# Performance work log

Hardware: AMD Instinct MI355X
Metric: run time of the kernel (lower is better)

Reference implementation:

```python
import jax, jax.numpy as jnp
import numpy as np

EPS = 1e-5

def _ln(x, g, b):
    m = jnp.mean(x, axis=-1, keepdims=True)
    v = jnp.var(x, axis=-1, keepdims=True)
    return (x - m) / jnp.sqrt(v + EPS) * g + b

def _mha(q, k, v, Wqkv, bqkv, Wo, bo, nh):
    # torch nn.MultiheadAttention with packed in_proj: rows [0:D]=Q, [D:2D]=K, [2D:3D]=V
    D = q.shape[-1]; hd = D // nh
    qp = q @ Wqkv[:D].T + bqkv[:D]
    kp = k @ Wqkv[D:2 * D].T + bqkv[D:2 * D]
    vp = v @ Wqkv[2 * D:].T + bqkv[2 * D:]
    sh = lambda t: t.reshape(t.shape[0], t.shape[1], nh, hd).transpose(0, 2, 1, 3)
    scores = jnp.einsum('bhqd,bhkd->bhqk', sh(qp), sh(kp)) / np.float32(np.sqrt(hd))
    a = jax.nn.softmax(scores, axis=-1)
    o = jnp.einsum('bhqk,bhkd->bhqd', a, sh(vp)).transpose(0, 2, 1, 3).reshape(q.shape[0], q.shape[1], D)
    return o @ Wo.T + bo

def _forward(x, W_in, b_in, W_l, b_l, g_l, be_l, W_ih, W_hh, b_ih, b_hh, mem0,
             W_rh, b_rh, W_wh, b_wh, W_eh, b_eh, W_rg, b_rg, W_wg, b_wg,
             W_wm_qkv, b_wm_qkv, W_wm_o, b_wm_o, W_ca_qkv, b_ca_qkv, W_ca_o, b_ca_o,
             W_ai, b_ai, g_ca, be_ca, W_out, b_out):
    B, S, _ = x.shape
    H = W_in.shape[0]
    # input projection + residual MLP stack (eval mode: dropout is identity)
    h = x @ W_in.T + b_in
    for i in range(W_l.shape[0]):
        r = h
        h = _ln(jax.nn.relu(h @ W_l[i].T + b_l[i]), g_l[i], be_l[i])
        h = h + r  # use_residual=True
    # working-memory (NTM-style) scan over time
    Hd = H

    def step(carry, xt):
        hs, cs, mem = carry
        gates = xt @ W_ih.T + b_ih + hs @ W_hh.T + b_hh
        i_, f_, g_, o_ = jnp.split(gates, 4, axis=-1)  # torch LSTM gate order i,f,g,o
        cs = jax.nn.sigmoid(f_) * cs + jax.nn.sigmoid(i_) * jnp.tanh(g_)
        hs = jax.nn.sigmoid(o_) * jnp.tanh(cs)
        # read (attention over memory, then gate)
        rk = hs @ W_rh.T + b_rh
        ro = _mha(rk[:, None, :], mem, mem, W_wm_qkv, b_wm_qkv, W_wm_o, b_wm_o, 4)
        rg = jax.nn.sigmoid(hs @ W_rg.T + b_rg)  # [B,1]
        read = (rg[:, :, None] * ro)[:, 0]
        # write (erase + add with content-based addressing, unscaled bmm softmax)
        wp = hs @ W_wh.T + b_wh
        wk, wv = wp[:, :Hd], wp[:, Hd:]
        ev = jax.nn.sigmoid(hs @ W_eh.T + b_eh)
        wg = jax.nn.sigmoid(hs @ W_wg.T + b_wg)  # [B,1]
        att = jax.nn.softmax(jnp.einsum('bd,bmd->bm', wk, mem), axis=-1)
        ew = att[:, :, None]  # [B,M,1]
        mem = mem * (1.0 - ew * ev[:, None, :]) + wg[:, None, :] * (ew * wv[:, None, :])
        return (hs, cs, mem), xt + read

    mem_init = jnp.broadcast_to(mem0, (B,) + mem0.shape)
    init = (jnp.zeros((B, H), x.dtype), jnp.zeros((B, H), x.dtype), mem_init)
    _, outs = jax.lax.scan(step, init, h.transpose(1, 0, 2))
    wm = outs.transpose(1, 0, 2)  # [B,S,H]
    # cognitive attention, task_type='general' (no task modulation branch)
    att = _mha(wm, wm, wm, W_ca_qkv, b_ca_qkv, W_ca_o, b_ca_o, 8)
    inten = jax.nn.sigmoid(wm @ W_ai.T + b_ai)
    co = _ln(att * inten + wm, g_ca, be_ca)
    return co @ W_out.T + b_out

def setup_inputs():
    key = jax.random.key(0)
    ks = iter(jax.random.split(key, 40))
    B, S, DI, H, DO, L, M = 16, 512, 64, 128, 64, 3, 32
    w = lambda *s: jax.random.normal(next(ks), s, jnp.float32) * 0.05
    d = {}
    d['x'] = jax.random.normal(next(ks), (B, S, DI), jnp.float32)
    d['W_in'] = w(H, DI); d['b_in'] = jnp.zeros(H)
    d['W_l'] = w(L, H, H); d['b_l'] = jnp.zeros((L, H))
    d['g_l'] = jnp.ones((L, H)); d['be_l'] = jnp.zeros((L, H))
    d['W_ih'] = w(4 * H, H); d['W_hh'] = w(4 * H, H)
    d['b_ih'] = jnp.zeros(4 * H); d['b_hh'] = jnp.zeros(4 * H)
    d['mem0'] = w(M, H)
    d['W_rh'] = w(H, H); d['b_rh'] = jnp.zeros(H)
    d['W_wh'] = w(2 * H, H); d['b_wh'] = jnp.zeros(2 * H)
    d['W_eh'] = w(H, H); d['b_eh'] = jnp.zeros(H)
    d['W_rg'] = w(1, H); d['b_rg'] = jnp.zeros(1)
    d['W_wg'] = w(1, H); d['b_wg'] = jnp.zeros(1)
    d['W_wm_qkv'] = w(3 * H, H); d['b_wm_qkv'] = jnp.zeros(3 * H)
    d['W_wm_o'] = w(H, H); d['b_wm_o'] = jnp.zeros(H)
    d['W_ca_qkv'] = w(3 * H, H); d['b_ca_qkv'] = jnp.zeros(3 * H)
    d['W_ca_o'] = w(H, H); d['b_ca_o'] = jnp.zeros(H)
    d['W_ai'] = w(1, H); d['b_ai'] = jnp.zeros(1)
    d['g_ca'] = jnp.ones(H); d['be_ca'] = jnp.zeros(H)
    d['W_out'] = w(DO, H); d['b_out'] = jnp.zeros(DO)
    return d

def reference(x, W_in, b_in, W_l, b_l, g_l, be_l, W_ih, W_hh, b_ih, b_hh, mem0,
              W_rh, b_rh, W_wh, b_wh, W_eh, b_eh, W_rg, b_rg, W_wg, b_wg,
              W_wm_qkv, b_wm_qkv, W_wm_o, b_wm_o, W_ca_qkv, b_ca_qkv, W_ca_o, b_ca_o,
              W_ai, b_ai, g_ca, be_ca, W_out, b_out):
    return _forward(x, W_in, b_in, W_l, b_l, g_l, be_l, W_ih, W_hh, b_ih, b_hh, mem0,
                    W_rh, b_rh, W_wh, b_wh, W_eh, b_eh, W_rg, b_rg, W_wg, b_wg,
                    W_wm_qkv, b_wm_qkv, W_wm_o, b_wm_o, W_ca_qkv, b_ca_qkv, W_ca_o, b_ca_o,
                    W_ai, b_ai, g_ca, be_ca, W_out, b_out)
```

## Files before the change

kernel.cpp:

```cpp
#include <hip/hip_runtime.h>
#include <hip/hip_bf16.h>


typedef short bf16x8 __attribute__((ext_vector_type(8)));
typedef float f32x4 __attribute__((ext_vector_type(4)));
typedef float f32x16 __attribute__((ext_vector_type(16)));

__device__ __forceinline__ float bl(uint u) { return __uint_as_float(u << 16); }
__device__ __forceinline__ float bh(uint u) { return __uint_as_float(u & 0xffff0000u); }
__device__ __forceinline__ float b2f(ushort u) { return __uint_as_float(((uint)u) << 16); }
__device__ __forceinline__ ushort f2b(float f) {
  uint u = __float_as_uint(f);
  u += 0x7fffu + ((u >> 16) & 1u);
  return (ushort)(u >> 16);
}
__device__ __forceinline__ uint cvtpk(float lo, float hi) {
  uint r;
  asm("v_cvt_pk_bf16_f32 %0, %1, %2" : "=v"(r) : "v"(lo), "v"(hi));
  return r;
}
__device__ __forceinline__ float rdl(float v, int lane) {
  return __int_as_float(__builtin_amdgcn_readlane(__float_as_int(v), lane));
}
__device__ __forceinline__ float sigm(float x) { return 1.0f / (1.0f + __expf(-x)); }
__device__ __forceinline__ float tanh_(float x) { float e = __expf(2.0f * x); return 1.0f - 2.0f / (e + 1.0f); }

__device__ __forceinline__ float dppror_add(float v, const int n) {
  int s;
  switch (n) {
    case 1: s = __builtin_amdgcn_update_dpp(0, __float_as_int(v), 0x121, 0xF, 0xF, true); break;
    case 2: s = __builtin_amdgcn_update_dpp(0, __float_as_int(v), 0x122, 0xF, 0xF, true); break;
    case 4: s = __builtin_amdgcn_update_dpp(0, __float_as_int(v), 0x124, 0xF, 0xF, true); break;
    default: s = __builtin_amdgcn_update_dpp(0, __float_as_int(v), 0x128, 0xF, 0xF, true); break;
  }
  return v + __int_as_float(s);
}
__device__ __forceinline__ float dppror_max(float v, const int n) {
  int s;
  switch (n) {
    case 1: s = __builtin_amdgcn_update_dpp(0, __float_as_int(v), 0x121, 0xF, 0xF, true); break;
    case 2: s = __builtin_amdgcn_update_dpp(0, __float_as_int(v), 0x122, 0xF, 0xF, true); break;
    case 4: s = __builtin_amdgcn_update_dpp(0, __float_as_int(v), 0x124, 0xF, 0xF, true); break;
    default: s = __builtin_amdgcn_update_dpp(0, __float_as_int(v), 0x128, 0xF, 0xF, true); break;
  }
  return fmaxf(v, __int_as_float(s));
}
__device__ __forceinline__ float swz16(float v) {
  return __int_as_float(__builtin_amdgcn_ds_swizzle(__float_as_int(v), 0x401F));
}
__device__ __forceinline__ float fold32_add(float v) {
  int a = __float_as_int(v), b = a;
  asm("v_permlane32_swap_b32 %0, %1" : "+v"(a), "+v"(b));
  return __int_as_float(a) + __int_as_float(b);
}

#define O_H     ((size_t)0)
#define O_GX    ((size_t)1048576)
#define O_EW    ((size_t)1048576)
#define O_QCA   ((size_t)1048576)
#define O_KCA   ((size_t)2097152)
#define O_VCA   ((size_t)3145728)
#define O_AO    ((size_t)4194304)
#define O_HS    ((size_t)5242880)
#define O_WM    ((size_t)5242880)
#define O_ST    ((size_t)6291456)
#define O_Q     ((size_t)9437184)
#define O_WGS   ((size_t)10485760)
#define O_RGS   ((size_t)10493952)
#define O_BQC   ((size_t)10502144)
#define O_MEMA  ((size_t)10502272)
#define O_PWIN  ((size_t)27279488)
#define O_PWL   ((size_t)27283584)
#define O_PWIH  ((size_t)27308160)
#define O_PCMB  ((size_t)27340928)
#define O_PQKV  ((size_t)27373696)
#define O_PWOC  ((size_t)27398272)
#define O_PWOUT ((size_t)27406464)
#define O_PWOWM ((size_t)27410688)
#define O_WQC16 ((size_t)27418880)
#define O_CAN   ((size_t)27427072)

#define F4LD(DST, OFS, P) { float4 _f = *(const float4*)(P); DST[(OFS)]=_f.x; DST[(OFS)+1]=_f.y; DST[(OFS)+2]=_f.z; DST[(OFS)+3]=_f.w; }

struct CV { const void* src; uint dst; uint n; };
struct CVA { CV d[36]; };
__global__ __launch_bounds__(256) void k_cvt(CVA a, ushort* cb)
{
  __shared__ int flag;
  int tid = threadIdx.x;
  const ushort* xu = (const ushort*)a.d[0].src;
  if (tid < 64) {
    int sane = 0;
    for (int i = tid; i < 512; i += 64) {
      int e = (xu[2 * i] >> 7) & 0xFF;
      sane += (e >= 0x70 && e <= 0x8E) ? 1 : 0;
    }
#pragma unroll
    for (int d = 1; d < 64; d <<= 1) sane += __shfl_xor(sane, d, 64);
    if (tid == 0) flag = (sane > 256) ? 0 : 1;
  }
  __syncthreads();
  int isf32 = flag;
  CV c = a.d[blockIdx.x];
  ushort* dst = cb + c.dst;
  uint start = blockIdx.y * 256 + tid, stride = gridDim.y * 256;
  if (isf32) {
    const float* s = (const float*)c.src;
    for (uint j = start; j < c.n; j += stride) dst[j] = f2b(s[j]);
  } else {
    const ushort* s = (const ushort*)c.src;
    for (uint j = start; j < c.n; j += stride) dst[j] = s[j];
  }
}

__global__ __launch_bounds__(256) void k_wqcomb(const ushort* __restrict__ Wqkv, const ushort* __restrict__ Wrh,
                                                const ushort* __restrict__ brh, const ushort* __restrict__ bqkv,
                                                ushort* __restrict__ wqc, float* __restrict__ bqc)
{
  __shared__ float qr[2][128];
  int tid = threadIdx.x;
  int r = tid >> 7, e = tid & 127;
  int j = blockIdx.x * 2 + r;
  qr[r][e] = b2f(Wqkv[j * 128 + e]);
  __syncthreads();
  float acc = 0.f;
  for (int k = 0; k < 128; ++k) acc += qr[r][k] * b2f(Wrh[k * 128 + e]);
  wqc[j * 128 + e] = f2b(acc);
  if (e == 0) {
    float s = 0.f;
    for (int k = 0; k < 128; ++k) s += qr[r][k] * b2f(brh[k]);
    bqc[j] = s + b2f(bqkv[j]);
  }
}

struct PD { const ushort* src; uint* dst; int R, C2, RT, base; };
struct PA { PD d[12]; };
__global__ __launch_bounds__(256) void k_pack(PA a)
{
  int p = blockIdx.x >> 5, sl = blockIdx.x & 31;
  PD q = a.d[p];
  for (int d2 = sl; d2 < q.C2; d2 += 32)
    for (int j = threadIdx.x; j < q.R; j += 256)
      q.dst[(size_t)d2 * q.RT + q.base + j] = *(const uint*)(q.src + (size_t)j * q.C2 * 2 + d2 * 2);
}

__device__ __forceinline__ void mlp_layer(float& h0, float& h1, const uint* wp, const float* bias, int li, int l)
{
  float t0 = bias[(1 + li) * 128 + l], t1 = bias[(1 + li) * 128 + 64 + l];
#pragma unroll
  for (int d2 = 0; d2 < 64; ++d2) {
    float s0 = rdl(d2 < 32 ? h0 : h1, (2 * d2) & 63);
    float s1 = rdl(d2 < 32 ? h0 : h1, (2 * d2 + 1) & 63);
    uint u0 = wp[d2 * 128 + l], u1 = wp[d2 * 128 + 64 + l];
    t0 += s0 * bl(u0) + s1 * bh(u0);
    t1 += s0 * bl(u1) + s1 * bh(u1);
  }
  t0 = fmaxf(t0, 0.f); t1 = fmaxf(t1, 0.f);
  float sm = t0 + t1, sq = t0 * t0 + t1 * t1;
#pragma unroll
  for (int d = 1; d < 64; d <<= 1) { sm += __shfl_xor(sm, d, 64); sq += __shfl_xor(sq, d, 64); }
  float mn = sm * 0.0078125f;
  float var = sq * 0.0078125f - mn * mn;
  float rstd = rsqrtf(var + 1e-5f);
  float ng0 = bias[(4 + li) * 128 + l], ng1 = bias[(4 + li) * 128 + 64 + l];
  float nb0 = bias[(7 + li) * 128 + l], nb1 = bias[(7 + li) * 128 + 64 + l];
  h0 = (t0 - mn) * rstd * ng0 + nb0 + h0;
  h1 = (t1 - mn) * rstd * ng1 + nb1 + h1;
}

__global__ __launch_bounds__(256, 1) void k_mlp(const ushort* __restrict__ x, const uint* __restrict__ pk,
    const ushort* __restrict__ b_in, const ushort* __restrict__ b_l, const ushort* __restrict__ g_l,
    const ushort* __restrict__ be_l, float* __restrict__ h_all)
{
  __shared__ uint lds[12288];
  __shared__ float bias[1280];
  int tid = threadIdx.x;
  for (int i = tid; i < 12288; i += 256) lds[i] = pk[i];
  for (int i = tid; i < 1280; i += 256) {
    int which = i >> 7, e = i & 127;
    float v;
    if (which == 0) v = b2f(b_in[e]);
    else if (which < 4) v = b2f(b_l[(which - 1) * 128 + e]);
    else if (which < 7) v = b2f(g_l[(which - 4) * 128 + e]);
    else v = b2f(be_l[(which - 7) * 128 + e]);
    bias[i] = v;
  }
  __syncthreads();
  int wv = tid >> 6, l = tid & 63;
  float h0a[8], h1a[8];
#pragma unroll
  for (int ps = 0; ps < 8; ++ps) {
    int tok = blockIdx.x * 32 + ps * 4 + wv;
    float xv = b2f(x[(size_t)tok * 64 + l]);
    float h0 = bias[l], h1 = bias[64 + l];
#pragma unroll
    for (int d2 = 0; d2 < 32; ++d2) {
      float s0 = rdl(xv, 2 * d2), s1 = rdl(xv, 2 * d2 + 1);
      uint u0 = lds[d2 * 128 + l], u1 = lds[d2 * 128 + 64 + l];
      h0 += s0 * bl(u0) + s1 * bh(u0);
      h1 += s0 * bl(u1) + s1 * bh(u1);
    }
    mlp_layer(h0, h1, lds + 4096, bias, 0, l);
    h0a[ps] = h0; h1a[ps] = h1;
  }
  __syncthreads();
  for (int i = tid; i < 8192; i += 256) lds[i] = pk[12288 + i];
  __syncthreads();
#pragma unroll
  for (int ps = 0; ps < 8; ++ps) {
    float h0 = h0a[ps], h1 = h1a[ps];
    mlp_layer(h0, h1, lds, bias, 1, l);
    h0a[ps] = h0; h1a[ps] = h1;
  }
  __syncthreads();
  for (int i = tid; i < 8192; i += 256) lds[i] = pk[20480 + i];
  __syncthreads();
#pragma unroll
  for (int ps = 0; ps < 8; ++ps) {
    int tok = blockIdx.x * 32 + ps * 4 + wv;
    float h0 = h0a[ps], h1 = h1a[ps];
    mlp_layer(h0, h1, lds, bias, 2, l);
    h_all[(size_t)tok * 128 + l] = h0;
    h_all[(size_t)tok * 128 + 64 + l] = h1;
  }
}

__global__ __launch_bounds__(256, 1) void k_gates(const float* __restrict__ h_all, const uint* __restrict__ pk,
    const ushort* __restrict__ b_ih, const ushort* __restrict__ b_hh, float* __restrict__ gx)
{
  __shared__ uint lds[8192];
  __shared__ float biasg[512];
  int tid = threadIdx.x;
  for (int i = tid; i < 512; i += 256) biasg[i] = b2f(b_ih[i]) + b2f(b_hh[i]);
  int wv = tid >> 6, l = tid & 63;
  for (int s = 0; s < 4; ++s) {
    __syncthreads();
    for (int i = tid; i < 8192; i += 256) { int d2 = i >> 7, j = i & 127; lds[i] = pk[d2 * 512 + s * 128 + j]; }
    __syncthreads();
    for (int ps = 0; ps < 8; ++ps) {
      int tok = blockIdx.x * 32 + ps * 4 + wv;
      float h0 = h_all[(size_t)tok * 128 + l], h1 = h_all[(size_t)tok * 128 + 64 + l];
      float a0 = biasg[s * 128 + l], a1 = biasg[s * 128 + 64 + l];
#pragma unroll
      for (int d2 = 0; d2 < 64; ++d2) {
        float s0 = rdl(d2 < 32 ? h0 : h1, (2 * d2) & 63);
        float s1 = rdl(d2 < 32 ? h0 : h1, (2 * d2 + 1) & 63);
        uint u0 = lds[d2 * 128 + l], u1 = lds[d2 * 128 + 64 + l];
        a0 += s0 * bl(u0) + s1 * bh(u0);
        a1 += s0 * bl(u1) + s1 * bh(u1);
      }
      gx[(size_t)tok * 512 + s * 128 + l] = a0;
      gx[(size_t)tok * 512 + s * 128 + 64 + l] = a1;
    }
  }
}

__global__ __launch_bounds__(512, 2) void k_lstm(const float* __restrict__ gx, const ushort* __restrict__ Whh,
                                                 float* __restrict__ hs_all)
{
  __shared__ float hsl[128];
  __shared__ float gact[512];
  int tid = threadIdx.x;
  int b = blockIdx.x;
  float2 w2[64];
  {
    const ushort* rp = Whh + (size_t)tid * 128;
#pragma unroll
    for (int q = 0; q < 16; ++q) {
      uint4 v = *(const uint4*)(rp + q * 8);
      w2[q * 4 + 0] = make_float2(bl(v.x), bh(v.x));
      w2[q * 4 + 1] = make_float2(bl(v.y), bh(v.y));
      w2[q * 4 + 2] = make_float2(bl(v.z), bh(v.z));
      w2[q * 4 + 3] = make_float2(bl(v.w), bh(v.w));
    }
  }
  if (tid < 128) hsl[tid] = 0.f;
  float cs = 0.f;
  const float* gbase = gx + (size_t)b * 512 * 512;
  float gcur = gbase[tid];
  int grp = tid >> 7;
  __syncthreads();
  for (int t = 0; t < 512; ++t) {
    float gnext = 0.f;
    if (t < 511) gnext = gbase[(size_t)(t + 1) * 512 + tid];
    float ax = gcur, ay = 0.f;
#pragma unroll
    for (int i = 0; i < 64; ++i) {
      float2 s2 = *(const float2*)(hsl + 2 * i);
      ax = fmaf(w2[i].x, s2.x, ax);
      ay = fmaf(w2[i].y, s2.y, ay);
    }
    float a = ax + ay;
    gact[tid] = (grp == 2) ? tanh_(a) : sigm(a);
    __syncthreads();
    if (tid < 128) {
      float si = gact[tid], sf = gact[128 + tid], tg = gact[256 + tid], so = gact[384 + tid];
      cs = sf * cs + si * tg;
      float hv = so * tanh_(cs);
      hsl[tid] = hv;
      hs_all[((size_t)b * 512 + t) * 128 + tid] = hv;
    }
    gcur = gnext;
    __syncthreads();
  }
}

__global__ __launch_bounds__(256, 1) void k_proj(const float* __restrict__ hs_all, const uint* __restrict__ pk,
    const ushort* __restrict__ bwh, const ushort* __restrict__ beh, const float* __restrict__ bqc,
    const ushort* __restrict__ wrg, const ushort* __restrict__ brg, const ushort* __restrict__ wwg,
    const ushort* __restrict__ bwg,
    float* __restrict__ st, float* __restrict__ q_a, float* __restrict__ rg_a)
{
  __shared__ uint lds[8192];
  __shared__ float biasc[512];
  int tid = threadIdx.x;
  for (int i = tid; i < 512; i += 256)
    biasc[i] = (i < 256) ? b2f(bwh[i]) : (i < 384) ? b2f(beh[i - 256]) : bqc[i - 384];
  float brgv = b2f(brg[0]), bwgv = b2f(bwg[0]);
  int wv = tid >> 6, l = tid & 63;
  for (int s = 0; s < 4; ++s) {
    __syncthreads();
    for (int i = tid; i < 8192; i += 256) { int d2 = i >> 7, j = i & 127; lds[i] = pk[d2 * 512 + s * 128 + j]; }
    __syncthreads();
    for (int ps = 0; ps < 8; ++ps) {
      int tok = blockIdx.x * 32 + ps * 4 + wv;
      float h0 = hs_all[(size_t)tok * 128 + l], h1 = hs_all[(size_t)tok * 128 + 64 + l];
      float a0 = biasc[s * 128 + l], a1 = biasc[s * 128 + 64 + l];
#pragma unroll
      for (int d2 = 0; d2 < 64; ++d2) {
        float s0 = rdl(d2 < 32 ? h0 : h1, (2 * d2) & 63);
        float s1 = rdl(d2 < 32 ? h0 : h1, (2 * d2 + 1) & 63);
        uint u0 = lds[d2 * 128 + l], u1 = lds[d2 * 128 + 64 + l];
        a0 += s0 * bl(u0) + s1 * bh(u0);
        a1 += s0 * bl(u1) + s1 * bh(u1);
      }
      if (s == 0) {
        st[(size_t)tok * 384 + l] = a0;
        st[(size_t)tok * 384 + 64 + l] = a1;
        float pr = h0 * b2f(wrg[l]) + h1 * b2f(wrg[64 + l]);
#pragma unroll
        for (int d = 1; d < 64; d <<= 1) pr += __shfl_xor(pr, d, 64);
        if (l == 0) rg_a[tok] = sigm(pr + brgv);
      } else if (s == 1) {
        float pw = h0 * b2f(wwg[l]) + h1 * b2f(wwg[64 + l]);
#pragma unroll
        for (int d = 1; d < 64; d <<= 1) pw += __shfl_xor(pw, d, 64);
        float wg = sigm(pw + bwgv);
        st[(size_t)tok * 384 + 256 + l] = wg * a0;
        st[(size_t)tok * 384 + 256 + 64 + l] = wg * a1;
      } else if (s == 2) {
        st[(size_t)tok * 384 + 128 + l] = sigm(a0);
        st[(size_t)tok * 384 + 128 + 64 + l] = sigm(a1);
      } else {
        q_a[(size_t)tok * 128 + l] = a0;
        q_a[(size_t)tok * 128 + 64 + l] = a1;
      }
    }
  }
}

__global__ __launch_bounds__(64, 1) void k_memrec(const float* __restrict__ st, const ushort* __restrict__ mem0,
    float* __restrict__ ew_all)
{
  __shared__ __align__(16) float sbuf[2][384];
  int l = threadIdx.x;
  int b = blockIdx.x;
  int r = l & 31, h = l >> 5;
  f32x16 mA, mB, mC, mD;
  {
    const uint* m0 = (const uint*)mem0 + r * 64 + 32 * h;
    uint4 uq;
#define LD16(V, OFS) \
    uq = *(const uint4*)(m0 + (OFS)); \
    V[0]=bl(uq.x); V[1]=bh(uq.x); V[2]=bl(uq.y); V[3]=bh(uq.y); \
    V[4]=bl(uq.z); V[5]=bh(uq.z); V[6]=bl(uq.w); V[7]=bh(uq.w); \
    uq = *(const uint4*)(m0 + (OFS) + 4); \
    V[8]=bl(uq.x); V[9]=bh(uq.x); V[10]=bl(uq.y); V[11]=bh(uq.y); \
    V[12]=bl(uq.z); V[13]=bh(uq.z); V[14]=bl(uq.w); V[15]=bh(uq.w);
    LD16(mA, 0) LD16(mB, 8) LD16(mC, 16) LD16(mD, 24)
#undef LD16
  }
  const float* stb = st + (size_t)b * 512 * 384;
  {
    float4 a = *(const float4*)(stb + 4 * l);
    float2 c = *(const float2*)(stb + 256 + 2 * l);
    *(float4*)(&sbuf[0][4 * l]) = a;
    *(float2*)(&sbuf[0][256 + 2 * l]) = c;
  }
  float moff = 0.f;
  float* ewp = ew_all + (size_t)b * 512 * 32 + r;
  for (int t = 0; t < 512; ++t) {
    int cur = t & 1, nxt = cur ^ 1;
    float4 ga = make_float4(0.f, 0.f, 0.f, 0.f);
    float2 gc = make_float2(0.f, 0.f);
    if (t < 511) {
      const float* sp = stb + (size_t)(t + 1) * 384;
      ga = *(const float4*)(sp + 4 * l);
      gc = *(const float2*)(sp + 256 + 2 * l);
    }
    const float* wkp = &sbuf[cur][h * 64];
    float dx = 0.f, dy = 0.f, dz = 0.f, dw = 0.f;
    float4 w4;
#define DOT4(V, J0, OFS) \
    w4 = *(const float4*)(wkp + (OFS)); \
    dx = fmaf(w4.x, V[(J0)+0], dx); dy = fmaf(w4.y, V[(J0)+1], dy); \
    dz = fmaf(w4.z, V[(J0)+2], dz); dw = fmaf(w4.w, V[(J0)+3], dw);
    DOT4(mA, 0, 0)  DOT4(mA, 4, 4)  DOT4(mA, 8, 8)   DOT4(mA, 12, 12)
    DOT4(mB, 0, 16) DOT4(mB, 4, 20) DOT4(mB, 8, 24)  DOT4(mB, 12, 28)
    DOT4(mC, 0, 32) DOT4(mC, 4, 36) DOT4(mC, 8, 40)  DOT4(mC, 12, 44)
    DOT4(mD, 0, 48) DOT4(mD, 4, 52) DOT4(mD, 8, 56)  DOT4(mD, 12, 60)
#undef DOT4
    float dp = (dx + dy) + (dz + dw);
    dp = fold32_add(dp);
    float e = __expf(dp - moff);
    float s16 = dppror_add(dppror_add(dppror_add(dppror_add(e, 1), 2), 4), 8);
    float den = s16 + swz16(s16);
    float ew = e / den;
    float x16 = dppror_max(dppror_max(dppror_max(dppror_max(dp, 1), 2), 4), 8);
    const float* evp = &sbuf[cur][128 + h * 64];
    const float* gvp = &sbuf[cur][256 + h * 64];
    float4 e4, g4;
#define UPD4(V, J0, OFS) \
    e4 = *(const float4*)(evp + (OFS)); g4 = *(const float4*)(gvp + (OFS)); \
    V[(J0)+0] = fmaf(ew, fmaf(-e4.x, V[(J0)+0], g4.x), V[(J0)+0]); \
    V[(J0)+1] = fmaf(ew, fmaf(-e4.y, V[(J0)+1], g4.y), V[(J0)+1]); \
    V[(J0)+2] = fmaf(ew, fmaf(-e4.z, V[(J0)+2], g4.z), V[(J0)+2]); \
    V[(J0)+3] = fmaf(ew, fmaf(-e4.w, V[(J0)+3], g4.w), V[(J0)+3]);
    UPD4(mA, 0, 0)  UPD4(mA, 4, 4)  UPD4(mA, 8, 8)   UPD4(mA, 12, 12)
    UPD4(mB, 0, 16) UPD4(mB, 4, 20) UPD4(mB, 8, 24)  UPD4(mB, 12, 28)
    UPD4(mC, 0, 32) UPD4(mC, 4, 36) UPD4(mC, 8, 40)  UPD4(mC, 12, 44)
    UPD4(mD, 0, 48) UPD4(mD, 4, 52) UPD4(mD, 8, 56)  UPD4(mD, 12, 60)
#undef UPD4
    if (t < 511) {
      *(float4*)(&sbuf[nxt][4 * l]) = ga;
      *(float2*)(&sbuf[nxt][256 + 2 * l]) = gc;
    }
    if (l < 32) ewp[(size_t)t * 32] = ew;
    moff = fmaxf(x16, swz16(x16));
  }
}

__global__ __launch_bounds__(256, 1) void k_snap(const float* __restrict__ st, const float* __restrict__ ew_all,
    const ushort* __restrict__ mem0, uint* __restrict__ mem_all)
{
  int b = blockIdx.x >> 3;
  int j = ((blockIdx.x & 7) << 8) + threadIdx.x;
  int m = j >> 6, d2 = j & 63;
  uint u0 = ((const uint*)mem0)[(m << 6) + d2];
  float s0 = bl(u0), s1 = bh(u0);
  const float* ep = st + (size_t)b * 512 * 384 + 128 + 2 * d2;
  const float* gp = ep + 128;
  const float* ap = ew_all + (size_t)b * 512 * 32 + m;
  uint* mb = mem_all + (size_t)b * 512 * 2048 + (m << 6) + d2;
  for (int t = 0; t < 512; t += 4) {
    float2 eA = *(const float2*)(ep + (size_t)(t + 0) * 384);
    float2 eB = *(const float2*)(ep + (size_t)(t + 1) * 384);
    float2 eC = *(const float2*)(ep + (size_t)(t + 2) * 384);
    float2 eD = *(const float2*)(ep + (size_t)(t + 3) * 384);
    float2 gA = *(const float2*)(gp + (size_t)(t + 0) * 384);
    float2 gB = *(const float2*)(gp + (size_t)(t + 1) * 384);
    float2 gC = *(const float2*)(gp + (size_t)(t + 2) * 384);
    float2 gD = *(const float2*)(gp + (size_t)(t + 3) * 384);
    float a0 = ap[(size_t)(t + 0) * 32];
    float a1 = ap[(size_t)(t + 1) * 32];
    float a2 = ap[(size_t)(t + 2) * 32];
    float a3 = ap[(size_t)(t + 3) * 32];
    mb[(size_t)(t + 0) * 2048] = cvtpk(s0, s1);
    s0 = fmaf(a0, fmaf(-eA.x, s0, gA.x), s0);
    s1 = fmaf(a0, fmaf(-eA.y, s1, gA.y), s1);
    mb[(size_t)(t + 1) * 2048] = cvtpk(s0, s1);
    s0 = fmaf(a1, fmaf(-eB.x, s0, gB.x), s0);
    s1 = fmaf(a1, fmaf(-eB.y, s1, gB.y), s1);
    mb[(size_t)(t + 2) * 2048] = cvtpk(s0, s1);
    s0 = fmaf(a2, fmaf(-eC.x, s0, gC.x), s0);
    s1 = fmaf(a2, fmaf(-eC.y, s1, gC.y), s1);
    mb[(size_t)(t + 3) * 2048] = cvtpk(s0, s1);
    s0 = fmaf(a3, fmaf(-eD.x, s0, gD.x), s0);
    s1 = fmaf(a3, fmaf(-eD.y, s1, gD.y), s1);
  }
}

__global__ __launch_bounds__(256, 1) void k_read(const ushort* __restrict__ Wqkv, const ushort* __restrict__ bwo,
    const uint* __restrict__ wo_pk, const uint* __restrict__ mem_all, const float* __restrict__ q_all,
    const float* __restrict__ rg_all, const float* __restrict__ h_all, float* __restrict__ wm_all)
{
  __shared__ float Kl[32 * 133];
  __shared__ float Vl[32 * 133];
  __shared__ __align__(16) char ml[8192];
  __shared__ float ql[128];
  __shared__ float ol[128];
  __shared__ float part[256];
  int tid = threadIdx.x, l = tid & 63, w = tid >> 6;
  int b = blockIdx.x >> 6, c = blockIdx.x & 63;
  int mat = w >> 1, chh = w & 1;
  bf16x8 bfr[4][4];
#pragma unroll
  for (int ct = 0; ct < 4; ++ct)
#pragma unroll
    for (int kt = 0; kt < 4; ++kt) {
      int j = chh * 64 + ct * 16 + (l & 15);
      bfr[ct][kt] = *(const bf16x8*)(Wqkv + (size_t)(128 + mat * 128 + j) * 128 + kt * 32 + (l >> 4) * 8);
    }
  for (int s8 = 0; s8 < 8; ++s8) {
    int t = c * 8 + s8;
    size_t bt = (size_t)b * 512 + t;
    {
      const uint4* src = (const uint4*)(mem_all + bt * 2048);
      uint4 v0 = src[tid * 2], v1 = src[tid * 2 + 1];
      int row = tid >> 3;
      int b0 = row * 256 + (tid & 7) * 32;
      int sw = (row & 7) << 4;
      *(uint4*)(ml + (b0 ^ sw)) = v0;
      *(uint4*)(ml + ((b0 + 16) ^ sw)) = v1;
    }
    if (tid < 128) ql[tid] = q_all[bt * 128 + tid];
    __syncthreads();
    f32x4 acc[2][4];
#pragma unroll
    for (int rt = 0; rt < 2; ++rt)
#pragma unroll
      for (int ct = 0; ct < 4; ++ct) { f32x4 z = {0.f, 0.f, 0.f, 0.f}; acc[rt][ct] = z; }
    bf16x8 af[2][4];
#pragma unroll
    for (int rt = 0; rt < 2; ++rt)
#pragma unroll
      for (int kt = 0; kt < 4; ++kt) {
        int row = rt * 16 + (l & 15);
        int byte0 = (row * 256 + kt * 64 + (l >> 4) * 16) ^ ((row & 7) << 4);
        af[rt][kt] = *(const bf16x8*)(ml + byte0);
      }
#pragma unroll
    for (int rt = 0; rt < 2; ++rt)
#pragma unroll
      for (int ct = 0; ct < 4; ++ct)
#pragma unroll
        for (int kt = 0; kt < 4; ++kt)
          acc[rt][ct] = __builtin_amdgcn_mfma_f32_16x16x32_bf16(af[rt][kt], bfr[ct][kt], acc[rt][ct], 0, 0, 0);
    {
      float* dst = mat ? Vl : Kl;
#pragma unroll
      for (int rt = 0; rt < 2; ++rt)
#pragma unroll
        for (int ct = 0; ct < 4; ++ct)
#pragma unroll
          for (int rr = 0; rr < 4; ++rr) {
            int row = rt * 16 + (l >> 4) * 4 + rr;
            int col = chh * 64 + ct * 16 + (l & 15);
            dst[row * 133 + col] = acc[rt][ct][rr];
          }
    }
    __syncthreads();
    {
      int hh = w;
      float qv[16];
#pragma unroll
      for (int q = 0; q < 4; ++q) { F4LD(qv, 4 * q, ql + hh * 32 + (l >> 5) * 16 + 4 * q); }
      int m = l & 31;
      float sv = 0.f;
#pragma unroll
      for (int i = 0; i < 16; ++i) sv += qv[i] * Kl[m * 133 + hh * 32 + (l >> 5) * 16 + i];
      sv += __shfl_xor(sv, 32, 64);
      sv *= 0.1767766952966369f;
      float mx = sv;
      mx = fmaxf(mx, __shfl_xor(mx, 1, 64)); mx = fmaxf(mx, __shfl_xor(mx, 2, 64));
      mx = fmaxf(mx, __shfl_xor(mx, 4, 64)); mx = fmaxf(mx, __shfl_xor(mx, 8, 64));
      mx = fmaxf(mx, __shfl_xor(mx, 16, 64));
      float e = __expf(sv - mx);
      float den = e;
      den += __shfl_xor(den, 1, 64); den += __shfl_xor(den, 2, 64); den += __shfl_xor(den, 4, 64);
      den += __shfl_xor(den, 8, 64); den += __shfl_xor(den, 16, 64);
      float a = e / den;
      float o = 0.f;
      int dpos = l & 31, mh = l >> 5;
#pragma unroll
      for (int i = 0; i < 16; ++i) {
        int mm = mh * 16 + i;
        float am = __shfl(a, mm, 64);
        o += am * Vl[mm * 133 + hh * 32 + dpos];
      }
      o += __shfl_xor(o, 32, 64);
      if (l < 32) ol[hh * 32 + dpos] = o;
    }
    __syncthreads();
    {
      int j = tid & 127, dh = tid >> 7;
      float o0 = ol[l], o1 = ol[64 + l];
      float pa = 0.f;
#pragma unroll
      for (int i2 = 0; i2 < 32; ++i2) {
        int d2 = dh * 32 + i2;
        float s0, s1;
        if (dh == 0) { s0 = rdl(o0, 2 * i2); s1 = rdl(o0, 2 * i2 + 1); }
        else { s0 = rdl(o1, 2 * i2); s1 = rdl(o1, 2 * i2 + 1); }
        uint u = wo_pk[d2 * 128 + j];
        pa += s0 * bl(u) + s1 * bh(u);
      }
      part[tid] = pa;
    }
    __syncthreads();
    if (tid < 128) {
      float ro = part[tid] + part[tid + 128] + b2f(bwo[tid]);
      float rg = rg_all[bt];
      wm_all[bt * 128 + tid] = h_all[bt * 128 + tid] + rg * ro;
    }
    __syncthreads();
  }
}

__global__ __launch_bounds__(256, 1) void k_caqkv(const float* __restrict__ wm, const uint* __restrict__ pk,
    const ushort* __restrict__ bqkv, float* __restrict__ qca, float* __restrict__ kca, float* __restrict__ vca)
{
  __shared__ uint lds[8192];
  int tid = threadIdx.x;
  int wv = tid >> 6, l = tid & 63;
  for (int s = 0; s < 3; ++s) {
    __syncthreads();
    for (int i = tid; i < 8192; i += 256) { int d2 = i >> 7, j = i & 127; lds[i] = pk[d2 * 384 + s * 128 + j]; }
    __syncthreads();
    for (int ps = 0; ps < 8; ++ps) {
      int tok = blockIdx.x * 32 + ps * 4 + wv;
      int b = tok >> 9, ss = tok & 511;
      float h0 = wm[(size_t)tok * 128 + l], h1 = wm[(size_t)tok * 128 + 64 + l];
      float a0 = b2f(bqkv[s * 128 + l]), a1 = b2f(bqkv[s * 128 + 64 + l]);
#pragma unroll
      for (int d2 = 0; d2 < 64; ++d2) {
        float s0 = rdl(d2 < 32 ? h0 : h1, (2 * d2) & 63);
        float s1 = rdl(d2 < 32 ? h0 : h1, (2 * d2 + 1) & 63);
        uint u0 = lds[d2 * 128 + l], u1 = lds[d2 * 128 + 64 + l];
        a0 += s0 * bl(u0) + s1 * bh(u0);
        a1 += s0 * bl(u1) + s1 * bh(u1);
      }
#pragma unroll
      for (int k = 0; k < 2; ++k) {
        int j = l + 64 * k;
        int hd = j >> 4, dd = j & 15;
        size_t idx = ((size_t)(b * 8 + hd) * 512 + ss) * 16 + dd;
        float v = k == 0 ? a0 : a1;
        if (s == 0) qca[idx] = v * 0.25f;
        else if (s == 1) kca[idx] = v;
        else vca[idx] = v;
      }
    }
  }
}

__global__ __launch_bounds__(256, 1) void k_caattn(const float* __restrict__ qca, const float* __restrict__ kca,
    const float* __restrict__ vca, float* __restrict__ ao)
{
  __shared__ float kl[8192];
  __shared__ uint vl[4096];
  int tid = threadIdx.x;
  int bh_ = blockIdx.x >> 1, half = blockIdx.x & 1;
  for (int i = tid; i < 8192; i += 256) kl[i] = kca[(size_t)bh_ * 8192 + i];
  for (int i = tid; i < 4096; i += 256) {
    float v0 = vca[(size_t)bh_ * 8192 + 2 * i], v1 = vca[(size_t)bh_ * 8192 + 2 * i + 1];
    vl[i] = (uint)f2b(v0) | ((uint)f2b(v1) << 16);
  }
  __syncthreads();
  int r = half * 256 + tid;
  float qv[16];
#pragma unroll
  for (int q = 0; q < 4; ++q) { F4LD(qv, 4 * q, qca + (size_t)bh_ * 8192 + r * 16 + 4 * q); }
  float o[16];
#pragma unroll
  for (int i = 0; i < 16; ++i) o[i] = 0.f;
  float mx = -3e38f, den = 0.f;
  for (int ch = 0; ch < 8; ++ch) {
    float sc[64];
#pragma unroll
    for (int m2 = 0; m2 < 64; ++m2) {
      const float* kr = kl + (ch * 64 + m2) * 16;
      float s = 0.f;
#pragma unroll
      for (int i = 0; i < 16; ++i) s += qv[i] * kr[i];
      sc[m2] = s;
    }
    float cm = sc[0];
#pragma unroll
    for (int m2 = 1; m2 < 64; ++m2) cm = fmaxf(cm, sc[m2]);
    if (cm > mx) {
      float rs = __expf(mx - cm);
      den *= rs;
#pragma unroll
      for (int i = 0; i < 16; ++i) o[i] *= rs;
      mx = cm;
    }
#pragma unroll
    for (int m2 = 0; m2 < 64; ++m2) {
      float e = __expf(sc[m2] - mx);
      den += e;
      const uint* vr = vl + (ch * 64 + m2) * 8;
#pragma unroll
      for (int i = 0; i < 8; ++i) {
        uint u = vr[i];
        o[2 * i] += e * bl(u);
        o[2 * i + 1] += e * bh(u);
      }
    }
  }
  float rd = 1.f / den;
#pragma unroll
  for (int q = 0; q < 4; ++q) {
    float4 f = make_float4(o[4 * q] * rd, o[4 * q + 1] * rd, o[4 * q + 2] * rd, o[4 * q + 3] * rd);
    *(float4*)(ao + (size_t)bh_ * 8192 + r * 16 + 4 * q) = f;
  }
}

__global__ __launch_bounds__(256, 1) void k_cafinal(const float* __restrict__ wm, const float* __restrict__ ao,
    const uint* __restrict__ pko, const uint* __restrict__ pkout,
    const ushort* __restrict__ wai, const ushort* __restrict__ bai, const ushort* __restrict__ gca,
    const ushort* __restrict__ beca, const ushort* __restrict__ boca, const ushort* __restrict__ bout,
    float* __restrict__ out)
{
  __shared__ uint lds[12288];
  __shared__ float fb[576];
  int tid = threadIdx.x;
  for (int i = tid; i < 8192; i += 256) lds[i] = pko[i];
  for (int i = tid; i < 4096; i += 256) lds[8192 + i] = pkout[i];
  for (int i = tid; i < 576; i += 256) {
    float v;
    if (i < 128) v = b2f(wai[i]);
    else if (i < 256) v = b2f(gca[i - 128]);
    else if (i < 384) v = b2f(beca[i - 256]);
    else if (i < 512) v = b2f(boca[i - 384]);
    else v = b2f(bout[i - 512]);
    fb[i] = v;
  }
  __syncthreads();
  float baiv = b2f(bai[0]);
  int wv = tid >> 6, l = tid & 63;
  for (int ps = 0; ps < 8; ++ps) {
    int tok = blockIdx.x * 32 + ps * 4 + wv;
    int b = tok >> 9, s = tok & 511;
    float w0 = wm[(size_t)tok * 128 + l], w1 = wm[(size_t)tok * 128 + 64 + l];
    float o0 = ao[((size_t)(b * 8 + (l >> 4)) * 512 + s) * 16 + (l & 15)];
    float o1 = ao[((size_t)(b * 8 + 4 + (l >> 4)) * 512 + s) * 16 + (l & 15)];
    float ip = w0 * fb[l] + w1 * fb[64 + l];
#pragma unroll
    for (int d = 1; d < 64; d <<= 1) ip += __shfl_xor(ip, d, 64);
    float it = sigm(ip + baiv);
    float a0 = fb[384 + l], a1 = fb[384 + 64 + l];
#pragma unroll
    for (int d2 = 0; d2 < 64; ++d2) {
      float s0 = rdl(d2 < 32 ? o0 : o1, (2 * d2) & 63);
      float s1 = rdl(d2 < 32 ? o0 : o1, (2 * d2 + 1) & 63);
      uint u0 = lds[d2 * 128 + l], u1 = lds[d2 * 128 + 64 + l];
      a0 += s0 * bl(u0) + s1 * bh(u0);
      a1 += s0 * bl(u1) + s1 * bh(u1);
    }
    float x0 = a0 * it + w0, x1 = a1 * it + w1;
    float smv = x0 + x1, sq = x0 * x0 + x1 * x1;
#pragma unroll
    for (int d = 1; d < 64; d <<= 1) { smv += __shfl_xor(smv, d, 64); sq += __shfl_xor(sq, d, 64); }
    float mn = smv * 0.0078125f;
    float var = sq * 0.0078125f - mn * mn;
    float rstd = rsqrtf(var + 1e-5f);
    float c0 = (x0 - mn) * rstd * fb[128 + l] + fb[256 + l];
    float c1 = (x1 - mn) * rstd * fb[128 + 64 + l] + fb[256 + 64 + l];
    float ob = fb[512 + l];
#pragma unroll
    for (int d2 = 0; d2 < 64; ++d2) {
      float s0 = rdl(d2 < 32 ? c0 : c1, (2 * d2) & 63);
      float s1 = rdl(d2 < 32 ? c0 : c1, (2 * d2 + 1) & 63);
      uint u = lds[8192 + d2 * 64 + l];
      ob += s0 * bl(u) + s1 * bh(u);
    }
    out[(size_t)tok * 64 + l] = ob;
  }
}

extern "C" void kernel_launch(void* const* d_in, const int* in_sizes, int n_in,
                              void* d_out, int out_size, void* d_ws, size_t ws_size,
                              hipStream_t stream)
{
  (void)out_size; (void)ws_size;
  float* ws = (float*)d_ws;
  uint* wsu = (uint*)d_ws;
  ushort* cb = (ushort*)(wsu + O_CAN);

  uint off[36]; uint cum = 0;
  for (int i = 0; i < 36; ++i) { off[i] = cum; cum = (cum + (uint)in_sizes[i] + 7u) & ~7u; }

  CVA ca;
  for (int i = 0; i < 36; ++i) ca.d[i] = CV{ d_in[i], off[i], (uint)in_sizes[i] };
  k_cvt<<<dim3(36, 16), 256, 0, stream>>>(ca, cb);

  const ushort* x        = cb + off[0];
  const ushort* W_in     = cb + off[1];
  const ushort* b_in     = cb + off[2];
  const ushort* W_l      = cb + off[3];
  const ushort* b_l      = cb + off[4];
  const ushort* g_l      = cb + off[5];
  const ushort* be_l     = cb + off[6];
  const ushort* W_ih     = cb + off[7];
  const ushort* W_hh     = cb + off[8];
  const ushort* b_ih     = cb + off[9];
  const ushort* b_hh     = cb + off[10];
  const ushort* mem0     = cb + off[11];
  const ushort* W_rh     = cb + off[12];
  const ushort* b_rh     = cb + off[13];
  const ushort* W_wh     = cb + off[14];
  const ushort* b_wh     = cb + off[15];
  const ushort* W_eh     = cb + off[16];
  const ushort* b_eh     = cb + off[17];
  const ushort* W_rg     = cb + off[18];
  const ushort* b_rg     = cb + off[19];
  const ushort* W_wg     = cb + off[20];
  const ushort* b_wg     = cb + off[21];
  const ushort* W_wm_qkv = cb + off[22];
  const ushort* b_wm_qkv = cb + off[23];
  const ushort* W_wm_o   = cb + off[24];
  const ushort* b_wm_o   = cb + off[25];
  const ushort* W_ca_qkv = cb + off[26];
  const ushort* b_ca_qkv = cb + off[27];
  const ushort* W_ca_o   = cb + off[28];
  const ushort* b_ca_o   = cb + off[29];
  const ushort* W_ai     = cb + off[30];
  const ushort* b_ai     = cb + off[31];
  const ushort* g_ca     = cb + off[32];
  const ushort* be_ca    = cb + off[33];
  const ushort* W_out    = cb + off[34];
  const ushort* b_out    = cb + off[35];

  k_wqcomb<<<64, 256, 0, stream>>>(W_wm_qkv, W_rh, b_rh, b_wm_qkv, (ushort*)(wsu + O_WQC16), ws + O_BQC);

  PA pa;
  pa.d[0]  = PD{ W_in,                       wsu + O_PWIN,  128, 32, 128, 0 };
  pa.d[1]  = PD{ W_l,                        wsu + O_PWL,   128, 64, 128, 0 };
  pa.d[2]  = PD{ W_l + 16384,                wsu + O_PWL + 8192,  128, 64, 128, 0 };
  pa.d[3]  = PD{ W_l + 32768,                wsu + O_PWL + 16384, 128, 64, 128, 0 };
  pa.d[4]  = PD{ W_ih,                       wsu + O_PWIH,  512, 64, 512, 0 };
  pa.d[5]  = PD{ W_wh,                       wsu + O_PCMB,  256, 64, 512, 0 };
  pa.d[6]  = PD{ W_eh,                       wsu + O_PCMB,  128, 64, 512, 256 };
  pa.d[7]  = PD{ (const ushort*)(wsu + O_WQC16), wsu + O_PCMB, 128, 64, 512, 384 };
  pa.d[8]  = PD{ W_ca_qkv,                   wsu + O_PQKV,  384, 64, 384, 0 };
  pa.d[9]  = PD{ W_ca_o,                     wsu + O_PWOC,  128, 64, 128, 0 };
  pa.d[10] = PD{ W_out,                      wsu + O_PWOUT,  64, 64,  64, 0 };
  pa.d[11] = PD{ W_wm_o,                     wsu + O_PWOWM, 128, 64, 128, 0 };
  k_pack<<<384, 256, 0, stream>>>(pa);

  k_mlp<<<256, 256, 0, stream>>>(x, wsu + O_PWIN, b_in, b_l, g_l, be_l, ws + O_H);
  k_gates<<<256, 256, 0, stream>>>(ws + O_H, wsu + O_PWIH, b_ih, b_hh, ws + O_GX);
  k_lstm<<<16, 512, 0, stream>>>(ws + O_GX, W_hh, ws + O_HS);
  k_proj<<<256, 256, 0, stream>>>(ws + O_HS, wsu + O_PCMB, b_wh, b_eh, ws + O_BQC,
                                  W_rg, b_rg, W_wg, b_wg,
                                  ws + O_ST, ws + O_Q, ws + O_RGS);
  k_memrec<<<16, 64, 0, stream>>>(ws + O_ST, mem0, ws + O_EW);
  k_snap<<<128, 256, 0, stream>>>(ws + O_ST, ws + O_EW, mem0, wsu + O_MEMA);
  k_read<<<1024, 256, 0, stream>>>(W_wm_qkv, b_wm_o, wsu + O_PWOWM, wsu + O_MEMA,
                                   ws + O_Q, ws + O_RGS, ws + O_H, ws + O_WM);
  k_caqkv<<<256, 256, 0, stream>>>(ws + O_WM, wsu + O_PQKV, b_ca_qkv, ws + O_QCA, ws + O_KCA, ws + O_VCA);
  k_caattn<<<256, 256, 0, stream>>>(ws + O_QCA, ws + O_KCA, ws + O_VCA, ws + O_AO);
  k_cafinal<<<256, 256, 0, stream>>>(ws + O_WM, ws + O_AO, wsu + O_PWOC, wsu + O_PWOUT,
                                     W_ai, b_ai, g_ca, be_ca, b_ca_o, b_out, (float*)d_out);
}
```

Before: 1.459 ms.

## Restructure LSTM recurrence to split-K quad reduction with one barrier per step

The LSTM step now gives each group of 4 lanes one hidden unit. Each lane computes partial dot products for all four gates over a 32-element slice of h, and the partials are combined with DPP quad shuffles. This removes the gate-activation LDS exchange and the second __syncthreads per timestep, and double-buffers the hidden state in LDS. A new pre-kernel rearranges W_hh into fp32 in the per-thread order the loop needs. The cost is an extra launch, more register pressure from 128 fp32 weights per thread, and every lane now evaluating all activations redundantly.

```diff
diff --git a/kernel.cpp b/kernel.cpp
--- a/kernel.cpp
+++ b/kernel.cpp
@@ -53,6 +53,12 @@
   asm("v_permlane32_swap_b32 %0, %1" : "+v"(a), "+v"(b));
   return __int_as_float(a) + __int_as_float(b);
 }
+__device__ __forceinline__ float qx1(float v) {
+  return __int_as_float(__builtin_amdgcn_update_dpp(0, __float_as_int(v), 0xB1, 0xF, 0xF, true));
+}
+__device__ __forceinline__ float qx2(float v) {
+  return __int_as_float(__builtin_amdgcn_update_dpp(0, __float_as_int(v), 0x4E, 0xF, 0xF, true));
+}
 
 #define O_H     ((size_t)0)
 #define O_GX    ((size_t)1048576)
@@ -61,6 +67,7 @@
 #define O_KCA   ((size_t)2097152)
 #define O_VCA   ((size_t)3145728)
 #define O_AO    ((size_t)4194304)
+#define O_WHF   ((size_t)4194304)
 #define O_HS    ((size_t)5242880)
 #define O_WM    ((size_t)5242880)
 #define O_ST    ((size_t)6291456)
@@ -144,6 +151,14 @@
       q.dst[(size_t)d2 * q.RT + q.base + j] = *(const uint*)(q.src + (size_t)j * q.C2 * 2 + d2 * 2);
 }
 
+__global__ __launch_bounds__(256) void k_whh(const ushort* __restrict__ Whh, float* __restrict__ whf)
+{
+  int e = blockIdx.x * 256 + threadIdx.x;
+  int j = e & 127, th = e >> 7;
+  int g = j >> 5, kk = j & 31, c = th >> 2, sl = th & 3;
+  whf[e] = b2f(Whh[(g * 128 + c) * 128 + sl * 32 + kk]);
+}
+
 __device__ __forceinline__ void mlp_layer(float& h0, float& h1, const uint* wp, const float* bias, int li, int l)
 {
   float t0 = bias[(1 + li) * 128 + l], t1 = bias[(1 + li) * 128 + 64 + l];
@@ -255,50 +270,60 @@
   }
 }
 
-__global__ __launch_bounds__(512, 2) void k_lstm(const float* __restrict__ gx, const ushort* __restrict__ Whh,
+__global__ __launch_bounds__(512, 2) void k_lstm(const float* __restrict__ gx, const float* __restrict__ whf,
                                                  float* __restrict__ hs_all)
 {
-  __shared__ float hsl[128];
-  __shared__ float gact[512];
+  __shared__ __align__(16) float hsl[2][128];
   int tid = threadIdx.x;
   int b = blockIdx.x;
-  float2 w2[64];
+  int s = tid & 3, c = tid >> 2;
+  f32x16 wA, wB, wC, wD, wE, wF, wG, wH;
   {
-    const ushort* rp = Whh + (size_t)tid * 128;
-#pragma unroll
-    for (int q = 0; q < 16; ++q) {
-      uint4 v = *(const uint4*)(rp + q * 8);
-      w2[q * 4 + 0] = make_float2(bl(v.x), bh(v.x));
-      w2[q * 4 + 1] = make_float2(bl(v.y), bh(v.y));
-      w2[q * 4 + 2] = make_float2(bl(v.z), bh(v.z));
-      w2[q * 4 + 3] = make_float2(bl(v.w), bh(v.w));
-    }
-  }
-  if (tid < 128) hsl[tid] = 0.f;
+    const float4* wp = (const float4*)(whf + (size_t)tid * 128);
+    float4 a0, a1, a2, a3;
+#define LW16(V, Q) \
+    a0 = wp[(Q)]; a1 = wp[(Q) + 1]; a2 = wp[(Q) + 2]; a3 = wp[(Q) + 3]; \
+    V[0]=a0.x; V[1]=a0.y; V[2]=a0.z; V[3]=a0.w; V[4]=a1.x; V[5]=a1.y; V[6]=a1.z; V[7]=a1.w; \
+    V[8]=a2.x; V[9]=a2.y; V[10]=a2.z; V[11]=a2.w; V[12]=a3.x; V[13]=a3.y; V[14]=a3.z; V[15]=a3.w;
+    LW16(wA, 0)  LW16(wB, 4)  LW16(wC, 8)  LW16(wD, 12)
+    LW16(wE, 16) LW16(wF, 20) LW16(wG, 24) LW16(wH, 28)
+#undef LW16
+  }
+  if (tid < 128) hsl[0][tid] = 0.f;
   float cs = 0.f;
-  const float* gbase = gx + (size_t)b * 512 * 512;
-  float gcur = gbase[tid];
-  int grp = tid >> 7;
+  const float* gbase = gx + (size_t)b * 512 * 512 + s * 128 + c;
+  float gcur = gbase[0];
+  float* hout = hs_all + (size_t)b * 512 * 128 + c;
   __syncthreads();
   for (int t = 0; t < 512; ++t) {
     float gnext = 0.f;
-    if (t < 511) gnext = gbase[(size_t)(t + 1) * 512 + tid];
-    float ax = gcur, ay = 0.f;
-#pragma unroll
-    for (int i = 0; i < 64; ++i) {
-      float2 s2 = *(const float2*)(hsl + 2 * i);
-      ax = fmaf(w2[i].x, s2.x, ax);
-      ay = fmaf(w2[i].y, s2.y, ay);
-    }
-    float a = ax + ay;
-    gact[tid] = (grp == 2) ? tanh_(a) : sigm(a);
-    __syncthreads();
-    if (tid < 128) {
-      float si = gact[tid], sf = gact[128 + tid], tg = gact[256 + tid], so = gact[384 + tid];
-      cs = sf * cs + si * tg;
-      float hv = so * tanh_(cs);
-      hsl[tid] = hv;
-      hs_all[((size_t)b * 512 + t) * 128 + tid] = hv;
+    if (t < 511) gnext = gbase[(size_t)(t + 1) * 512];
+    const float* hp = &hsl[t & 1][s * 32];
+    float p0 = (s == 0) ? gcur : 0.f;
+    float p1 = (s == 1) ? gcur : 0.f;
+    float p2 = (s == 2) ? gcur : 0.f;
+    float p3 = (s == 3) ? gcur : 0.f;
+    float4 h4;
+#define DOT4(V0, V1, V2, V3, J, HOFS) \
+    h4 = *(const float4*)(hp + (HOFS)); \
+    p0 = fmaf(V0[(J)+0], h4.x, p0); p0 = fmaf(V0[(J)+1], h4.y, p0); p0 = fmaf(V0[(J)+2], h4.z, p0); p0 = fmaf(V0[(J)+3], h4.w, p0); \
+    p1 = fmaf(V1[(J)+0], h4.x, p1); p1 = fmaf(V1[(J)+1], h4.y, p1); p1 = fmaf(V1[(J)+2], h4.z, p1); p1 = fmaf(V1[(J)+3], h4.w, p1); \
+    p2 = fmaf(V2[(J)+0], h4.x, p2); p2 = fmaf(V2[(J)+1], h4.y, p2); p2 = fmaf(V2[(J)+2], h4.z, p2); p2 = fmaf(V2[(J)+3], h4.w, p2); \
+    p3 = fmaf(V3[(J)+0], h4.x, p3); p3 = fmaf(V3[(J)+1], h4.y, p3); p3 = fmaf(V3[(J)+2], h4.z, p3); p3 = fmaf(V3[(J)+3], h4.w, p3);
+    DOT4(wA, wC, wE, wG, 0, 0)   DOT4(wA, wC, wE, wG, 4, 4)
+    DOT4(wA, wC, wE, wG, 8, 8)   DOT4(wA, wC, wE, wG, 12, 12)
+    DOT4(wB, wD, wF, wH, 0, 16)  DOT4(wB, wD, wF, wH, 4, 20)
+    DOT4(wB, wD, wF, wH, 8, 24)  DOT4(wB, wD, wF, wH, 12, 28)
+#undef DOT4
+    p0 += qx1(p0); p0 += qx2(p0);
+    p1 += qx1(p1); p1 += qx2(p1);
+    p2 += qx1(p2); p2 += qx2(p2);
+    p3 += qx1(p3); p3 += qx2(p3);
+    cs = sigm(p1) * cs + sigm(p0) * tanh_(p2);
+    float hv = sigm(p3) * tanh_(cs);
+    if (s == 0) {
+      hsl[(t + 1) & 1][c] = hv;
+      hout[(size_t)t * 128] = hv;
     }
     gcur = gnext;
     __syncthreads();
@@ -838,10 +863,11 @@
   pa.d[10] = PD{ W_out,                      wsu + O_PWOUT,  64, 64,  64, 0 };
   pa.d[11] = PD{ W_wm_o,                     wsu + O_PWOWM, 128, 64, 128, 0 };
   k_pack<<<384, 256, 0, stream>>>(pa);
+  k_whh<<<256, 256, 0, stream>>>(W_hh, ws + O_WHF);
 
   k_mlp<<<256, 256, 0, stream>>>(x, wsu + O_PWIN, b_in, b_l, g_l, be_l, ws + O_H);
   k_gates<<<256, 256, 0, stream>>>(ws + O_H, wsu + O_PWIH, b_ih, b_hh, ws + O_GX);
-  k_lstm<<<16, 512, 0, stream>>>(ws + O_GX, W_hh, ws + O_HS);
+  k_lstm<<<16, 512, 0, stream>>>(ws + O_GX, ws + O_WHF, ws + O_HS);
   k_proj<<<256, 256, 0, stream>>>(ws + O_HS, wsu + O_PCMB, b_wh, b_eh, ws + O_BQC,
                                   W_rg, b_rg, W_wg, b_wg,
                                   ws + O_ST, ws + O_Q, ws + O_RGS);
```

Measured after the change: 1.392 ms. -4.6%, faster.
